# Kernel optimization log

Measured on AMD Instinct MI355X. Metric: run time of the kernel, lower is better.

## Reference

```python
import jax, jax.numpy as jnp
from jax import lax
import numpy as np

B = 32768
H = 7
W = 7
EMB = 64
NUM_ACTIONS = 7
HIDDEN = 128
CNN_OUT = 64 * 3 * 3  # 576, from 7x7 input through the conv/pool stack


def setup_inputs() -> dict:
    key = jax.random.key(0)
    ks = jax.random.split(key, 20)
    frame = jax.random.randint(ks[0], (2, B, H, W, 3), 0, 11, dtype=jnp.int32)
    carried_col = jax.random.randint(ks[1], (2, B, 1), 0, 6, dtype=jnp.int32)
    carried_obj = jax.random.randint(ks[2], (2, B, 1), 0, 11, dtype=jnp.int32)

    def w(k, shape):
        return (jax.random.normal(k, shape, jnp.float32) * 0.05)

    return {
        "frame": frame,
        "carried_col": carried_col,
        "carried_obj": carried_obj,
        "conv1_w": w(ks[3], (16, 3, 2, 2)),  "conv1_b": jnp.zeros((16,), jnp.float32),
        "conv2_w": w(ks[4], (32, 16, 2, 2)), "conv2_b": jnp.zeros((32,), jnp.float32),
        "conv3_w": w(ks[5], (64, 32, 2, 2)), "conv3_b": jnp.zeros((64,), jnp.float32),
        "proj_w": w(ks[6], (EMB, CNN_OUT + 2)), "proj_b": jnp.zeros((EMB,), jnp.float32),
        "h1_w": w(ks[7], (HIDDEN, EMB * 2 + 4)), "h1_b": jnp.zeros((HIDDEN,), jnp.float32),
        "ln_g": jnp.ones((HIDDEN,), jnp.float32), "ln_b": jnp.zeros((HIDDEN,), jnp.float32),
        "h2_w": w(ks[8], (HIDDEN, HIDDEN)), "h2_b": jnp.zeros((HIDDEN,), jnp.float32),
        "h3_w": w(ks[9], (NUM_ACTIONS, HIDDEN)), "h3_b": jnp.zeros((NUM_ACTIONS,), jnp.float32),
    }


def _conv(x, wgt, b):
    # Conv2d(kernel=2, padding=1), NCHW
    y = lax.conv_general_dilated(x, wgt, (1, 1), [(1, 1), (1, 1)],
                                 dimension_numbers=("NCHW", "OIHW", "NCHW"))
    return y + b[None, :, None, None]


def _maxpool2(x):
    # MaxPool2d(2): window 2, stride 2, floor (VALID)
    return lax.reduce_window(x, -jnp.inf, lax.max, (1, 1, 2, 2), (1, 1, 2, 2), "VALID")


def _encode(fr, cc, co, p):
    x = fr.transpose(0, 3, 1, 2).astype(jnp.float32)  # [B,3,H,W]
    x = _maxpool2(jax.nn.relu(_conv(x, p["conv1_w"], p["conv1_b"])))  # [B,16,4,4]
    x = _maxpool2(jax.nn.relu(_conv(x, p["conv2_w"], p["conv2_b"])))  # [B,32,2,2]
    x = jax.nn.relu(_conv(x, p["conv3_w"], p["conv3_b"]))             # [B,64,3,3]
    feats = x.reshape(x.shape[0], -1)                                  # [B,576]
    carried = jnp.concatenate([cc, co], axis=-1).astype(jnp.float32)   # [B,2]
    comb = jnp.concatenate([feats, carried], axis=1)                   # [B,578]
    return jax.nn.relu(comb @ p["proj_w"].T + p["proj_b"])            # [B,64]


def _dir_pos(fr):
    # vectorized first-match of frame[...,0]==10 in row-major order
    b = fr.shape[0]
    mask = (fr[..., 0] == 10).reshape(b, -1)             # [B, H*W]
    has = jnp.any(mask, axis=-1)                         # [B]
    idx = jnp.argmax(mask, axis=-1)                      # first True (row-major)
    y = idx // W
    x = idx % W
    ch2 = fr[..., 2].reshape(b, -1)
    d_raw = jnp.take_along_axis(ch2, idx[:, None], axis=1)[:, 0] % 4
    d = jnp.where(has, d_raw, 0)                         # [B] int
    pos = jnp.stack([y.astype(jnp.float32) / (H - 1),
                     x.astype(jnp.float32) / (W - 1)], axis=-1)
    pos = jnp.where(has[:, None], pos, jnp.float32(0.5))  # [B,2]
    return d, pos


def _forward(frame, carried_col, carried_obj, p):
    curr_f, next_f = frame[0], frame[1]
    curr_emb = _encode(curr_f, carried_col[0], carried_obj[0], p)
    next_emb = _encode(next_f, carried_col[1], carried_obj[1], p)
    cd, cpos = _dir_pos(curr_f)
    nd, npos = _dir_pos(next_f)
    delta = ((nd - cd + 4) % 4).astype(jnp.float32)
    angle = delta * (2.0 * 3.14159 / 4.0)  # matches source constant
    dir_delta = jnp.stack([jnp.sin(angle), jnp.cos(angle)], axis=-1)  # [B,2]
    pos_delta = npos - cpos                                           # [B,2]
    comb = jnp.concatenate([curr_emb, next_emb, dir_delta, pos_delta], axis=-1)  # [B,132]
    h = comb @ p["h1_w"].T + p["h1_b"]
    mu = h.mean(-1, keepdims=True)
    var = ((h - mu) ** 2).mean(-1, keepdims=True)
    h = (h - mu) * lax.rsqrt(var + 1e-5) * p["ln_g"] + p["ln_b"]
    h = jax.nn.relu(h)  # dropout = identity in eval
    h = jax.nn.relu(h @ p["h2_w"].T + p["h2_b"])
    return h @ p["h3_w"].T + p["h3_b"]  # [B, num_actions]


def reference(frame, carried_col, carried_obj,
              conv1_w, conv1_b, conv2_w, conv2_b, conv3_w, conv3_b,
              proj_w, proj_b, h1_w, h1_b, ln_g, ln_b,
              h2_w, h2_b, h3_w, h3_b):
    p = dict(conv1_w=conv1_w, conv1_b=conv1_b, conv2_w=conv2_w, conv2_b=conv2_b,
             conv3_w=conv3_w, conv3_b=conv3_b, proj_w=proj_w, proj_b=proj_b,
             h1_w=h1_w, h1_b=h1_b, ln_g=ln_g, ln_b=ln_b,
             h2_w=h2_w, h2_b=h2_b, h3_w=h3_w, h3_b=h3_b)
    return _forward(frame, carried_col, carried_obj, p)
```

## Files before the change

### kernel.cpp

```cpp
#include <hip/hip_runtime.h>
#include <hip/hip_bf16.h>

#define BATCH 32768
#define NELEM 65536

typedef unsigned short u16;
typedef unsigned int u32;
typedef __attribute__((ext_vector_type(8))) short bf16x8;
typedef __attribute__((ext_vector_type(4))) float f32x4;

__device__ __forceinline__ float bf2f(u16 u) {
    union { u32 u; float f; } c; c.u = ((u32)u) << 16; return c.f;
}
__device__ __forceinline__ u16 f2bf(float f) {
    union { float f; u32 u; } c; c.f = f;
    u32 x = c.u;
    u32 r = (x + 0x7fffu + ((x >> 16) & 1u)) >> 16;
    return (u16)r;
}

__global__ __launch_bounds__(256) void k0_prep(const float* __restrict__ pw,
        const float* __restrict__ w2, const float* __restrict__ w3,
        const float* __restrict__ h2w, const float* __restrict__ h1w,
        const float* __restrict__ w1,
        u16* __restrict__ pwT, u16* __restrict__ w2r, u16* __restrict__ w3r,
        u16* __restrict__ h2hi, u16* __restrict__ h2lo,
        u16* __restrict__ h1hi, u16* __restrict__ h1lo,
        u16* __restrict__ w1hi, u16* __restrict__ w1lo) {
    int idx = blockIdx.x * 256 + threadIdx.x;
    if (idx < 38912) {
        int j = idx / 608, kk = idx - j * 608;
        float v = 0.f;
        if (kk < 576) {
            int p = kk >> 6, oc = kk & 63;
            v = pw[j * 578 + oc * 9 + p];
        } else if (kk < 578) {
            v = pw[j * 578 + kk];
        }
        pwT[idx] = f2bf(v);
    } else if (idx < 40960) {
        int i = idx - 38912;
        int oc = i >> 6, rem = i & 63, tap = rem >> 4, ic = rem & 15;
        w2r[i] = f2bf(w2[oc * 64 + ic * 4 + tap]);
    } else if (idx < 49152) {
        int i = idx - 40960;
        int oc = i >> 7, rem = i & 127, tap = rem >> 5, ic = rem & 31;
        w3r[i] = f2bf(w3[oc * 128 + ic * 4 + tap]);
    } else if (idx < 65536) {
        int i = idx - 49152;
        float v = h2w[i];
        u16 hi = f2bf(v);
        h2hi[i] = hi;
        h2lo[i] = f2bf(v - bf2f(hi));
    } else if (idx < 86016) {
        int i = idx - 65536;
        int j = i / 160, k = i - j * 160;
        float v = (k < 132) ? h1w[j * 132 + k] : 0.f;
        u16 hi = f2bf(v);
        h1hi[i] = hi;
        h1lo[i] = f2bf(v - bf2f(hi));
    } else if (idx < 86528) {
        int i = idx - 86016;
        int oc = i >> 5, k = i & 31;
        int ky = k >> 4, kx = (k >> 3) & 1, c = k & 7;
        float v = (c < 3) ? w1[oc * 12 + c * 4 + ky * 2 + kx] : 0.f;
        u16 hi = f2bf(v);
        w1hi[i] = hi;
        w1lo[i] = f2bf(v - bf2f(hi));
    }
}

__global__ __launch_bounds__(256) void kconv_all(const int* __restrict__ frame,
        const u16* __restrict__ w1hi, const u16* __restrict__ w1lo,
        const float* __restrict__ b1,
        const u16* __restrict__ w2r, const float* __restrict__ b2,
        const u16* __restrict__ w3r, const float* __restrict__ b3,
        const int* __restrict__ ccol, const int* __restrict__ cobj,
        const u16* __restrict__ pwT, const float* __restrict__ pb,
        float* __restrict__ comb) {
    __shared__ u16 lds[24576];
    u16* p2L   = lds;
    u16* p1L   = lds + 4096;
    u16* frL   = lds + 12288;
    u16* featL = lds + 4096;
    int t = threadIdx.x;
    int l = t & 63;
    int wv = t >> 6;
    int col = l & 15;
    int kg = l >> 4;
    int e0 = blockIdx.x * 32;

    #pragma unroll
    for (int i = 0; i < 6; ++i) {
        int o = i * 256 + t;
        if (o < 1312) *(uint4*)(frL + o * 8) = make_uint4(0u, 0u, 0u, 0u);
    }

    {
        bf16x8 c1hi = *(const bf16x8*)(w1hi + col * 32 + kg * 8);
        bf16x8 c1lo = *(const bf16x8*)(w1lo + col * 32 + kg * 8);
        float c1b = b1[col];
        int ky1 = kg >> 1, kx1 = kg & 1;
        bool wr1 = (kg < 2);
        for (int h = 0; h < 2; ++h) {
            __syncthreads();
            const int* fbase = frame + (size_t)(e0 + h * 16) * 147;
            #pragma unroll
            for (int i = 0; i < 10; ++i) {
                int idx = i * 256 + t;
                if (idx < 2352) {
                    int le = idx / 147, r = idx - le * 147;
                    int cell = r / 3, c = r - cell * 3;
                    int y = cell / 7, x = cell - y * 7;
                    frL[le * 656 + (y + 1) * 72 + (x + 1) * 8 + c] = f2bf((float)fbase[idx]);
                }
            }
            __syncthreads();
            #pragma unroll
            for (int q = 0; q < 4; ++q) {
                int le = wv * 4 + q;
                const u16* eb = frL + le * 656;
                u16* op = p1L + (h * 16 + le) * 256;
                #pragma unroll
                for (int mt = 0; mt < 4; ++mt) {
                    int posA = mt * 16 + col;
                    int oy = posA >> 3, ox = posA & 7;
                    bf16x8 a = *(const bf16x8*)(eb + (oy + ky1) * 72 + (ox + kx1) * 8);
                    f32x4 acc = {0.f, 0.f, 0.f, 0.f};
                    acc = __builtin_amdgcn_mfma_f32_16x16x32_bf16(a, c1hi, acc, 0, 0, 0);
                    acc = __builtin_amdgcn_mfma_f32_16x16x32_bf16(a, c1lo, acc, 0, 0, 0);
                    float x0 = fmaxf(acc[0] + c1b, 0.f);
                    float x1 = fmaxf(acc[1] + c1b, 0.f);
                    float x2 = fmaxf(acc[2] + c1b, 0.f);
                    float x3 = fmaxf(acc[3] + c1b, 0.f);
                    float y0 = fmaxf(x0, x1);
                    float y1 = fmaxf(x2, x3);
                    float m0 = fmaxf(y0, __shfl_xor(y0, 32, 64));
                    float m1 = fmaxf(y1, __shfl_xor(y1, 32, 64));
                    if (wr1) {
                        op[(mt * 4 + kg * 2 + 0) * 16 + col] = f2bf(m0);
                        op[(mt * 4 + kg * 2 + 1) * 16 + col] = f2bf(m1);
                    }
                }
            }
        }
    }
    __syncthreads();

    {
        bf16x8 bfrag[2][2];
        #pragma unroll
        for (int s = 0; s < 2; ++s)
            #pragma unroll
            for (int nt = 0; nt < 2; ++nt)
                bfrag[s][nt] = *(const bf16x8*)(w2r + (nt * 16 + col) * 64 + s * 32 + kg * 8);
        float bias2[2] = { b2[col], b2[16 + col] };
        int oy = col >> 2, ox = col & 3;
        int aoff[2]; bool aok[2];
        #pragma unroll
        for (int s = 0; s < 2; ++s) {
            int tap = 2 * s + (kg >> 1);
            int ky = tap >> 1, kx = tap & 1;
            int iy = oy - 1 + ky, ix = ox - 1 + kx;
            aok[s] = (iy >= 0 && ix >= 0);
            aoff[s] = (iy * 4 + ix) * 16 + (kg & 1) * 8;
        }
        #pragma unroll
        for (int q = 0; q < 8; ++q) {
            int e = wv * 8 + q;
            const u16* pbase = p1L + e * 256;
            bf16x8 a0 = {0,0,0,0,0,0,0,0}, a1 = {0,0,0,0,0,0,0,0};
            if (aok[0]) a0 = *(const bf16x8*)(pbase + aoff[0]);
            if (aok[1]) a1 = *(const bf16x8*)(pbase + aoff[1]);
            f32x4 acc0 = {0.f,0.f,0.f,0.f}, acc1 = {0.f,0.f,0.f,0.f};
            acc0 = __builtin_amdgcn_mfma_f32_16x16x32_bf16(a0, bfrag[0][0], acc0, 0, 0, 0);
            acc1 = __builtin_amdgcn_mfma_f32_16x16x32_bf16(a0, bfrag[0][1], acc1, 0, 0, 0);
            acc0 = __builtin_amdgcn_mfma_f32_16x16x32_bf16(a1, bfrag[1][0], acc0, 0, 0, 0);
            acc1 = __builtin_amdgcn_mfma_f32_16x16x32_bf16(a1, bfrag[1][1], acc1, 0, 0, 0);
            #pragma unroll
            for (int nt = 0; nt < 2; ++nt) {
                f32x4 acc = nt ? acc1 : acc0;
                float b = bias2[nt];
                float m0 = fmaxf(fmaxf(acc[0] + b, 0.f), fmaxf(acc[1] + b, 0.f));
                float m1 = fmaxf(fmaxf(acc[2] + b, 0.f), fmaxf(acc[3] + b, 0.f));
                float p0 = fmaxf(m0, __shfl_xor(m0, 16, 64));
                float p1 = fmaxf(m1, __shfl_xor(m1, 16, 64));
                if ((kg & 1) == 0) {
                    int qq = (kg >> 1) * 2;
                    u16* op = p2L + e * 128 + nt * 16 + col;
                    op[qq * 32]       = f2bf(p0);
                    op[(qq + 1) * 32] = f2bf(p1);
                }
            }
        }
    }
    __syncthreads();

    int colhi = col >> 3, collo = col & 7;
    {
        bf16x8 bfrag[4][4];
        #pragma unroll
        for (int s = 0; s < 4; ++s)
            #pragma unroll
            for (int nt = 0; nt < 4; ++nt)
                bfrag[s][nt] = *(const bf16x8*)(w3r + (nt * 16 + col) * 128 + s * 32 + kg * 8);
        float bias[4];
        #pragma unroll
        for (int nt = 0; nt < 4; ++nt) bias[nt] = b3[nt * 16 + col];

        auto do_tile = [&](int i) {
            int m0 = i * 16;
            int m = m0 + col;
            u32 elem = (u32)(((unsigned long long)(u32)m * 954437177ull) >> 33);
            int p = m - (int)elem * 9;
            int oy = (p * 86) >> 8;
            int ox = p - 3 * oy;
            const u16* pbase = p2L + elem * 128 + kg * 8;
            f32x4 acc[4];
            #pragma unroll
            for (int nt = 0; nt < 4; ++nt) {
                acc[nt][0] = 0.f; acc[nt][1] = 0.f; acc[nt][2] = 0.f; acc[nt][3] = 0.f;
            }
            #pragma unroll
            for (int s = 0; s < 4; ++s) {
                int ky = s >> 1, kx = s & 1;
                int iy = oy - 1 + ky, ix = ox - 1 + kx;
                bf16x8 a = {0,0,0,0,0,0,0,0};
                if (iy >= 0 && iy <= 1 && ix >= 0 && ix <= 1)
                    a = *(const bf16x8*)(pbase + (iy * 2 + ix) * 32);
                #pragma unroll
                for (int nt = 0; nt < 4; ++nt)
                    acc[nt] = __builtin_amdgcn_mfma_f32_16x16x32_bf16(a, bfrag[s][nt], acc[nt], 0, 0, 0);
            }
            #pragma unroll
            for (int r = 0; r < 4; ++r) {
                int mr = m0 + kg * 4 + r;
                u32 er = (u32)(((unsigned long long)(u32)mr * 954437177ull) >> 33);
                int pr = mr - (int)er * 9;
                int e7 = (int)(er & 7u);
                u16* fb = featL + er * 640 + collo;
                #pragma unroll
                for (int nt = 0; nt < 4; ++nt) {
                    int blk = (pr * 8 + nt * 2 + colhi) ^ e7;
                    fb[blk * 8] = f2bf(fmaxf(acc[nt][r] + bias[nt], 0.f));
                }
            }
        };
        #pragma unroll
        for (int u = 0; u < 4; ++u) do_tile(wv + u * 4);
        if (wv < 2) do_tile(16 + wv);
    }
    if (t < 32) {
        union { u16 s[8]; uint4 q; } b;
        b.s[0] = f2bf((float)ccol[e0 + t]);
        b.s[1] = f2bf((float)cobj[e0 + t]);
        #pragma unroll
        for (int i = 2; i < 8; ++i) b.s[i] = 0;
        *(uint4*)(featL + t * 640 + (72 ^ (t & 7)) * 8) = b.q;
    }
    __syncthreads();

    int rh = wv & 1, nh = wv >> 1;
    int m0g = e0 + rh * 16;
    const u16* arowb = featL + (rh * 16 + col) * 640;
    int rx = col & 7;
    const u16* brow = pwT + (nh * 32 + col) * 608 + kg * 8;
    f32x4 acc0 = {0.f,0.f,0.f,0.f}, acc1 = {0.f,0.f,0.f,0.f};
    #pragma unroll
    for (int k0 = 0; k0 < 608; k0 += 32) {
        bf16x8 a;
        if (k0 + kg * 8 < 584) {
            int L = (k0 >> 3) + kg;
            a = *(const bf16x8*)(arowb + (L ^ rx) * 8);
        } else {
            #pragma unroll
            for (int j = 0; j < 8; ++j) a[j] = 0;
        }
        bf16x8 b0 = *(const bf16x8*)(brow + k0);
        bf16x8 b1 = *(const bf16x8*)(brow + 16 * 608 + k0);
        acc0 = __builtin_amdgcn_mfma_f32_16x16x32_bf16(a, b0, acc0, 0, 0, 0);
        acc1 = __builtin_amdgcn_mfma_f32_16x16x32_bf16(a, b1, acc1, 0, 0, 0);
    }
    float* outbase = (m0g < BATCH) ? (comb + (size_t)m0g * 160)
                                   : (comb + (size_t)(m0g - BATCH) * 160 + 64);
    #pragma unroll
    for (int nt = 0; nt < 2; ++nt) {
        int n = nh * 32 + nt * 16 + col;
        float pbv = pb[n];
        f32x4 acc = nt ? acc1 : acc0;
        #pragma unroll
        for (int r = 0; r < 4; ++r) {
            outbase[(kg * 4 + r) * 160 + n] = fmaxf(acc[r] + pbv, 0.f);
        }
    }
}

__global__ __launch_bounds__(256) void k5_extras(const int* __restrict__ frame,
        float* __restrict__ comb) {
    int b = blockIdx.x * 256 + threadIdx.x;
    int d[2]; float posy[2], posx[2];
    for (int f = 0; f < 2; ++f) {
        const int* fb = frame + (size_t)(f * BATCH + b) * 147;
        int idx = 49;
        for (int cell = 0; cell < 49; ++cell) {
            int v = fb[cell * 3];
            if (idx == 49 && v == 10) idx = cell;
        }
        if (idx < 49) {
            d[f] = fb[idx * 3 + 2] & 3;
            posy[f] = (float)(idx / 7) / 6.0f;
            posx[f] = (float)(idx % 7) / 6.0f;
        } else {
            d[f] = 0; posy[f] = 0.5f; posx[f] = 0.5f;
        }
    }
    int delta = (d[1] - d[0] + 4) & 3;
    const float ANG = (float)(2.0 * 3.14159 / 4.0);
    float angle = (float)delta * ANG;
    float4 o;
    o.x = sinf(angle);
    o.y = cosf(angle);
    o.z = posy[1] - posy[0];
    o.w = posx[1] - posx[0];
    float* cb = comb + (size_t)b * 160 + 128;
    *(float4*)cb = o;
    float4 z = make_float4(0.f, 0.f, 0.f, 0.f);
    #pragma unroll
    for (int i = 1; i < 8; ++i) *(float4*)(cb + i * 4) = z;
}

__device__ __forceinline__ void split8(const float* __restrict__ x,
                                       bf16x8& hi, bf16x8& lo) {
    #pragma unroll
    for (int j = 0; j < 8; ++j) {
        u16 h = f2bf(x[j]);
        hi[j] = (short)h;
        lo[j] = (short)f2bf(x[j] - bf2f(h));
    }
}

__global__ __launch_bounds__(256) void k6_h1_gemm(const float* __restrict__ in,
        const u16* __restrict__ whi, const u16* __restrict__ wlo,
        const float* __restrict__ bias, float* __restrict__ out) {
    int t = threadIdx.x;
    int l = t & 63;
    int col = l & 15;
    int kg = l >> 4;
    int m0 = blockIdx.x * 64 + (t >> 6) * 16;
    const float* arow = in + (size_t)(m0 + col) * 160 + kg * 8;
    const u16* bh = whi + col * 160 + kg * 8;
    const u16* bl = wlo + col * 160 + kg * 8;

    f32x4 acc[8];
    #pragma unroll
    for (int nt = 0; nt < 8; ++nt) {
        acc[nt][0] = 0.f; acc[nt][1] = 0.f; acc[nt][2] = 0.f; acc[nt][3] = 0.f;
    }
    #pragma unroll
    for (int s = 0; s < 5; ++s) {
        float x[8];
        #pragma unroll
        for (int j = 0; j < 8; ++j) x[j] = arow[s * 32 + j];
        bf16x8 ahi, alo;
        split8(x, ahi, alo);
        #pragma unroll
        for (int nt = 0; nt < 8; ++nt) {
            bf16x8 bhiF = *(const bf16x8*)(bh + nt * 2560 + s * 32);
            bf16x8 bloF = *(const bf16x8*)(bl + nt * 2560 + s * 32);
            acc[nt] = __builtin_amdgcn_mfma_f32_16x16x32_bf16(ahi, bhiF, acc[nt], 0, 0, 0);
            acc[nt] = __builtin_amdgcn_mfma_f32_16x16x32_bf16(alo, bhiF, acc[nt], 0, 0, 0);
            acc[nt] = __builtin_amdgcn_mfma_f32_16x16x32_bf16(ahi, bloF, acc[nt], 0, 0, 0);
        }
    }
    #pragma unroll
    for (int nt = 0; nt < 8; ++nt) {
        float bv = bias[nt * 16 + col];
        #pragma unroll
        for (int r = 0; r < 4; ++r) {
            int m = m0 + kg * 4 + r;
            out[m * 128 + nt * 16 + col] = acc[nt][r] + bv;
        }
    }
}

__global__ __launch_bounds__(256) void k6_ln(const float* __restrict__ h,
        const float* __restrict__ lng, const float* __restrict__ lnb,
        float* __restrict__ out) {
    int w = (blockIdx.x * 256 + threadIdx.x) >> 6;
    int l = threadIdx.x & 63;
    const float* row = h + (size_t)w * 128 + l * 2;
    float2 v = *(const float2*)row;
    float s = v.x + v.y;
    s += __shfl_xor(s, 1, 64);
    s += __shfl_xor(s, 2, 64);
    s += __shfl_xor(s, 4, 64);
    s += __shfl_xor(s, 8, 64);
    s += __shfl_xor(s, 16, 64);
    s += __shfl_xor(s, 32, 64);
    float mu = s * (1.0f / 128.0f);
    float d0 = v.x - mu, d1 = v.y - mu;
    float vs = d0 * d0 + d1 * d1;
    vs += __shfl_xor(vs, 1, 64);
    vs += __shfl_xor(vs, 2, 64);
    vs += __shfl_xor(vs, 4, 64);
    vs += __shfl_xor(vs, 8, 64);
    vs += __shfl_xor(vs, 16, 64);
    vs += __shfl_xor(vs, 32, 64);
    float rs = rsqrtf(vs * (1.0f / 128.0f) + 1e-5f);
    float2 o;
    o.x = fmaxf(d0 * rs * lng[l * 2]     + lnb[l * 2],     0.f);
    o.y = fmaxf(d1 * rs * lng[l * 2 + 1] + lnb[l * 2 + 1], 0.f);
    *(float2*)(out + (size_t)w * 128 + l * 2) = o;
}

__global__ __launch_bounds__(256) void k7_h2_mfma(const float* __restrict__ in,
        const u16* __restrict__ whi, const u16* __restrict__ wlo,
        const float* __restrict__ bias, float* __restrict__ out) {
    int t = threadIdx.x;
    int l = t & 63;
    int col = l & 15;
    int kg = l >> 4;
    int m0 = blockIdx.x * 64 + (t >> 6) * 16;
    const float* arow = in + (size_t)(m0 + col) * 128 + kg * 8;
    const u16* bh = whi + col * 128 + kg * 8;
    const u16* bl = wlo + col * 128 + kg * 8;

    f32x4 acc[8];
    #pragma unroll
    for (int nt = 0; nt < 8; ++nt) {
        acc[nt][0] = 0.f; acc[nt][1] = 0.f; acc[nt][2] = 0.f; acc[nt][3] = 0.f;
    }
    #pragma unroll
    for (int s = 0; s < 4; ++s) {
        float x[8];
        #pragma unroll
        for (int j = 0; j < 8; ++j) x[j] = arow[s * 32 + j];
        bf16x8 ahi, alo;
        split8(x, ahi, alo);
        #pragma unroll
        for (int nt = 0; nt < 8; ++nt) {
            bf16x8 bhiF = *(const bf16x8*)(bh + nt * 2048 + s * 32);
            bf16x8 bloF = *(const bf16x8*)(bl + nt * 2048 + s * 32);
            acc[nt] = __builtin_amdgcn_mfma_f32_16x16x32_bf16(ahi, bhiF, acc[nt], 0, 0, 0);
            acc[nt] = __builtin_amdgcn_mfma_f32_16x16x32_bf16(alo, bhiF, acc[nt], 0, 0, 0);
            acc[nt] = __builtin_amdgcn_mfma_f32_16x16x32_bf16(ahi, bloF, acc[nt], 0, 0, 0);
        }
    }
    #pragma unroll
    for (int nt = 0; nt < 8; ++nt) {
        float bv = bias[nt * 16 + col];
        #pragma unroll
        for (int r = 0; r < 4; ++r) {
            int m = m0 + kg * 4 + r;
            out[m * 128 + nt * 16 + col] = fmaxf(acc[nt][r] + bv, 0.f);
        }
    }
}

__global__ __launch_bounds__(256) void k8_h3(const float* __restrict__ in,
        const float* __restrict__ w, const float* __restrict__ bias,
        float* __restrict__ out) {
    int r = blockIdx.x * 256 + threadIdx.x;
    float acc[7];
    #pragma unroll
    for (int j = 0; j < 7; ++j) acc[j] = bias[j];
    const float* row = in + (size_t)r * 128;
    #pragma unroll 4
    for (int c = 0; c < 32; ++c) {
        float4 v = *(const float4*)(row + c * 4);
        #pragma unroll
        for (int j = 0; j < 7; ++j) {
            acc[j] += v.x * w[j * 128 + c * 4 + 0];
            acc[j] += v.y * w[j * 128 + c * 4 + 1];
            acc[j] += v.z * w[j * 128 + c * 4 + 2];
            acc[j] += v.w * w[j * 128 + c * 4 + 3];
        }
    }
    #pragma unroll
    for (int j = 0; j < 7; ++j) out[r * 7 + j] = acc[j];
}

extern "C" void kernel_launch(void* const* d_in, const int* in_sizes, int n_in,
                              void* d_out, int out_size, void* d_ws, size_t ws_size,
                              hipStream_t stream) {
    const int*   frame = (const int*)d_in[0];
    const int*   ccol  = (const int*)d_in[1];
    const int*   cobj  = (const int*)d_in[2];
    const float* w1    = (const float*)d_in[3];
    const float* b1    = (const float*)d_in[4];
    const float* w2    = (const float*)d_in[5];
    const float* b2    = (const float*)d_in[6];
    const float* w3    = (const float*)d_in[7];
    const float* b3    = (const float*)d_in[8];
    const float* pw    = (const float*)d_in[9];
    const float* pb    = (const float*)d_in[10];
    const float* h1w   = (const float*)d_in[11];
    const float* h1b   = (const float*)d_in[12];
    const float* lng   = (const float*)d_in[13];
    const float* lnb   = (const float*)d_in[14];
    const float* h2w   = (const float*)d_in[15];
    const float* h2b   = (const float*)d_in[16];
    const float* h3w   = (const float*)d_in[17];
    const float* h3b   = (const float*)d_in[18];
    float* out = (float*)d_out;

    char* ws = (char*)d_ws;
    float* comb     = (float*)(ws + 0);
    float* h1out    = (float*)(ws + 33554432);
    float* h2out    = (float*)(ws + 50331648);
    float* h1pre    = (float*)(ws + 95420416);
    u16*   pwT      = (u16*)(ws + 132120576);
    u16*   w2r      = (u16*)(ws + 132120576 + 131072);
    u16*   w3r      = (u16*)(ws + 132120576 + 139264);
    u16*   h2hi     = (u16*)(ws + 132120576 + 163840);
    u16*   h2lo     = (u16*)(ws + 132120576 + 196608);
    u16*   h1hi     = (u16*)(ws + 132120576 + 229376);
    u16*   h1lo     = (u16*)(ws + 132120576 + 270336);
    u16*   w1hi     = (u16*)(ws + 132120576 + 311296);
    u16*   w1lo     = (u16*)(ws + 132120576 + 312320);

    k0_prep<<<340, 256, 0, stream>>>(pw, w2, w3, h2w, h1w, w1,
                                     pwT, w2r, w3r, h2hi, h2lo, h1hi, h1lo,
                                     w1hi, w1lo);
    kconv_all<<<2048, 256, 0, stream>>>(frame, w1hi, w1lo, b1, w2r, b2,
                                        w3r, b3, ccol, cobj, pwT, pb, comb);
    k5_extras<<<128, 256, 0, stream>>>(frame, comb);
    k6_h1_gemm<<<512, 256, 0, stream>>>(comb, h1hi, h1lo, h1b, h1pre);
    k6_ln<<<8192, 256, 0, stream>>>(h1pre, lng, lnb, h1out);
    k7_h2_mfma<<<512, 256, 0, stream>>>(h1out, h2hi, h2lo, h2b, h2out);
    k8_h3<<<128, 256, 0, stream>>>(h2out, h3w, h3b, out);
}
```

Measured before the change: 255.9 us.

## Fuse h1 GEMM, LayerNorm, h2 GEMM and h3 head into one LDS-staged kernel

Replaces the four separate MLP-head kernels with a single kernel that keeps each 64-row tile in shared memory between stages. The h1 output, LayerNorm result and h2 output no longer round-trip through global memory, and three launches go away. In exchange the kernel holds about 33 KB of LDS per block and adds block barriers, which may lower occupancy. The final 7-wide head now runs on 4 threads per row, each computing two outputs.

```diff
diff --git a/kernel.cpp b/kernel.cpp
--- a/kernel.cpp
+++ b/kernel.cpp
@@ -339,145 +339,144 @@
     }
 }
 
-__global__ __launch_bounds__(256) void k6_h1_gemm(const float* __restrict__ in,
-        const u16* __restrict__ whi, const u16* __restrict__ wlo,
-        const float* __restrict__ bias, float* __restrict__ out) {
+__global__ __launch_bounds__(256) void kmlp(const float* __restrict__ comb,
+        const u16* __restrict__ h1hi, const u16* __restrict__ h1lo,
+        const float* __restrict__ h1b,
+        const float* __restrict__ lng, const float* __restrict__ lnb,
+        const u16* __restrict__ h2hi, const u16* __restrict__ h2lo,
+        const float* __restrict__ h2b,
+        const float* __restrict__ h3w, const float* __restrict__ h3b,
+        float* __restrict__ out) {
+    __shared__ float hL[64 * 132];
     int t = threadIdx.x;
     int l = t & 63;
     int col = l & 15;
     int kg = l >> 4;
-    int m0 = blockIdx.x * 64 + (t >> 6) * 16;
-    const float* arow = in + (size_t)(m0 + col) * 160 + kg * 8;
-    const u16* bh = whi + col * 160 + kg * 8;
-    const u16* bl = wlo + col * 160 + kg * 8;
-
-    f32x4 acc[8];
-    #pragma unroll
-    for (int nt = 0; nt < 8; ++nt) {
-        acc[nt][0] = 0.f; acc[nt][1] = 0.f; acc[nt][2] = 0.f; acc[nt][3] = 0.f;
-    }
-    #pragma unroll
-    for (int s = 0; s < 5; ++s) {
-        float x[8];
-        #pragma unroll
-        for (int j = 0; j < 8; ++j) x[j] = arow[s * 32 + j];
-        bf16x8 ahi, alo;
-        split8(x, ahi, alo);
+    int wv = t >> 6;
+    int mb = blockIdx.x * 64;
+
+    {
+        const float* arow = comb + (size_t)(mb + wv * 16 + col) * 160 + kg * 8;
+        const u16* bh = h1hi + col * 160 + kg * 8;
+        const u16* bl = h1lo + col * 160 + kg * 8;
+        f32x4 acc[8];
         #pragma unroll
         for (int nt = 0; nt < 8; ++nt) {
-            bf16x8 bhiF = *(const bf16x8*)(bh + nt * 2560 + s * 32);
-            bf16x8 bloF = *(const bf16x8*)(bl + nt * 2560 + s * 32);
-            acc[nt] = __builtin_amdgcn_mfma_f32_16x16x32_bf16(ahi, bhiF, acc[nt], 0, 0, 0);
-            acc[nt] = __builtin_amdgcn_mfma_f32_16x16x32_bf16(alo, bhiF, acc[nt], 0, 0, 0);
-            acc[nt] = __builtin_amdgcn_mfma_f32_16x16x32_bf16(ahi, bloF, acc[nt], 0, 0, 0);
-        }
-    }
-    #pragma unroll
-    for (int nt = 0; nt < 8; ++nt) {
-        float bv = bias[nt * 16 + col];
-        #pragma unroll
-        for (int r = 0; r < 4; ++r) {
-            int m = m0 + kg * 4 + r;
-            out[m * 128 + nt * 16 + col] = acc[nt][r] + bv;
-        }
-    }
-}
-
-__global__ __launch_bounds__(256) void k6_ln(const float* __restrict__ h,
-        const float* __restrict__ lng, const float* __restrict__ lnb,
-        float* __restrict__ out) {
-    int w = (blockIdx.x * 256 + threadIdx.x) >> 6;
-    int l = threadIdx.x & 63;
-    const float* row = h + (size_t)w * 128 + l * 2;
-    float2 v = *(const float2*)row;
-    float s = v.x + v.y;
-    s += __shfl_xor(s, 1, 64);
-    s += __shfl_xor(s, 2, 64);
-    s += __shfl_xor(s, 4, 64);
-    s += __shfl_xor(s, 8, 64);
-    s += __shfl_xor(s, 16, 64);
-    s += __shfl_xor(s, 32, 64);
-    float mu = s * (1.0f / 128.0f);
-    float d0 = v.x - mu, d1 = v.y - mu;
-    float vs = d0 * d0 + d1 * d1;
-    vs += __shfl_xor(vs, 1, 64);
-    vs += __shfl_xor(vs, 2, 64);
-    vs += __shfl_xor(vs, 4, 64);
-    vs += __shfl_xor(vs, 8, 64);
-    vs += __shfl_xor(vs, 16, 64);
-    vs += __shfl_xor(vs, 32, 64);
-    float rs = rsqrtf(vs * (1.0f / 128.0f) + 1e-5f);
-    float2 o;
-    o.x = fmaxf(d0 * rs * lng[l * 2]     + lnb[l * 2],     0.f);
-    o.y = fmaxf(d1 * rs * lng[l * 2 + 1] + lnb[l * 2 + 1], 0.f);
-    *(float2*)(out + (size_t)w * 128 + l * 2) = o;
-}
-
-__global__ __launch_bounds__(256) void k7_h2_mfma(const float* __restrict__ in,
-        const u16* __restrict__ whi, const u16* __restrict__ wlo,
-        const float* __restrict__ bias, float* __restrict__ out) {
-    int t = threadIdx.x;
-    int l = t & 63;
-    int col = l & 15;
-    int kg = l >> 4;
-    int m0 = blockIdx.x * 64 + (t >> 6) * 16;
-    const float* arow = in + (size_t)(m0 + col) * 128 + kg * 8;
-    const u16* bh = whi + col * 128 + kg * 8;
-    const u16* bl = wlo + col * 128 + kg * 8;
-
-    f32x4 acc[8];
-    #pragma unroll
-    for (int nt = 0; nt < 8; ++nt) {
-        acc[nt][0] = 0.f; acc[nt][1] = 0.f; acc[nt][2] = 0.f; acc[nt][3] = 0.f;
-    }
-    #pragma unroll
-    for (int s = 0; s < 4; ++s) {
-        float x[8];
-        #pragma unroll
-        for (int j = 0; j < 8; ++j) x[j] = arow[s * 32 + j];
-        bf16x8 ahi, alo;
-        split8(x, ahi, alo);
+            acc[nt][0] = 0.f; acc[nt][1] = 0.f; acc[nt][2] = 0.f; acc[nt][3] = 0.f;
+        }
+        #pragma unroll
+        for (int s = 0; s < 5; ++s) {
+            float x[8];
+            #pragma unroll
+            for (int j = 0; j < 8; ++j) x[j] = arow[s * 32 + j];
+            bf16x8 ahi, alo;
+            split8(x, ahi, alo);
+            #pragma unroll
+            for (int nt = 0; nt < 8; ++nt) {
+                bf16x8 bhiF = *(const bf16x8*)(bh + nt * 2560 + s * 32);
+                bf16x8 bloF = *(const bf16x8*)(bl + nt * 2560 + s * 32);
+                acc[nt] = __builtin_amdgcn_mfma_f32_16x16x32_bf16(ahi, bhiF, acc[nt], 0, 0, 0);
+                acc[nt] = __builtin_amdgcn_mfma_f32_16x16x32_bf16(alo, bhiF, acc[nt], 0, 0, 0);
+                acc[nt] = __builtin_amdgcn_mfma_f32_16x16x32_bf16(ahi, bloF, acc[nt], 0, 0, 0);
+            }
+        }
         #pragma unroll
         for (int nt = 0; nt < 8; ++nt) {
-            bf16x8 bhiF = *(const bf16x8*)(bh + nt * 2048 + s * 32);
-            bf16x8 bloF = *(const bf16x8*)(bl + nt * 2048 + s * 32);
-            acc[nt] = __builtin_amdgcn_mfma_f32_16x16x32_bf16(ahi, bhiF, acc[nt], 0, 0, 0);
-            acc[nt] = __builtin_amdgcn_mfma_f32_16x16x32_bf16(alo, bhiF, acc[nt], 0, 0, 0);
-            acc[nt] = __builtin_amdgcn_mfma_f32_16x16x32_bf16(ahi, bloF, acc[nt], 0, 0, 0);
-        }
-    }
-    #pragma unroll
-    for (int nt = 0; nt < 8; ++nt) {
-        float bv = bias[nt * 16 + col];
-        #pragma unroll
-        for (int r = 0; r < 4; ++r) {
-            int m = m0 + kg * 4 + r;
-            out[m * 128 + nt * 16 + col] = fmaxf(acc[nt][r] + bv, 0.f);
-        }
-    }
-}
-
-__global__ __launch_bounds__(256) void k8_h3(const float* __restrict__ in,
-        const float* __restrict__ w, const float* __restrict__ bias,
-        float* __restrict__ out) {
-    int r = blockIdx.x * 256 + threadIdx.x;
-    float acc[7];
-    #pragma unroll
-    for (int j = 0; j < 7; ++j) acc[j] = bias[j];
-    const float* row = in + (size_t)r * 128;
-    #pragma unroll 4
-    for (int c = 0; c < 32; ++c) {
-        float4 v = *(const float4*)(row + c * 4);
-        #pragma unroll
-        for (int j = 0; j < 7; ++j) {
-            acc[j] += v.x * w[j * 128 + c * 4 + 0];
-            acc[j] += v.y * w[j * 128 + c * 4 + 1];
-            acc[j] += v.z * w[j * 128 + c * 4 + 2];
-            acc[j] += v.w * w[j * 128 + c * 4 + 3];
-        }
-    }
-    #pragma unroll
-    for (int j = 0; j < 7; ++j) out[r * 7 + j] = acc[j];
+            float bv = h1b[nt * 16 + col];
+            #pragma unroll
+            for (int r = 0; r < 4; ++r)
+                hL[(wv * 16 + kg * 4 + r) * 132 + nt * 16 + col] = acc[nt][r] + bv;
+        }
+    }
+    __syncthreads();
+
+    for (int rr = 0; rr < 16; ++rr) {
+        float* rp = hL + (wv * 16 + rr) * 132 + l * 2;
+        float2 v = *(const float2*)rp;
+        float s = v.x + v.y;
+        s += __shfl_xor(s, 1, 64);
+        s += __shfl_xor(s, 2, 64);
+        s += __shfl_xor(s, 4, 64);
+        s += __shfl_xor(s, 8, 64);
+        s += __shfl_xor(s, 16, 64);
+        s += __shfl_xor(s, 32, 64);
+        float mu = s * (1.0f / 128.0f);
+        float d0 = v.x - mu, d1 = v.y - mu;
+        float vs = d0 * d0 + d1 * d1;
+        vs += __shfl_xor(vs, 1, 64);
+        vs += __shfl_xor(vs, 2, 64);
+        vs += __shfl_xor(vs, 4, 64);
+        vs += __shfl_xor(vs, 8, 64);
+        vs += __shfl_xor(vs, 16, 64);
+        vs += __shfl_xor(vs, 32, 64);
+        float rs = rsqrtf(vs * (1.0f / 128.0f) + 1e-5f);
+        float2 o;
+        o.x = fmaxf(d0 * rs * lng[l * 2]     + lnb[l * 2],     0.f);
+        o.y = fmaxf(d1 * rs * lng[l * 2 + 1] + lnb[l * 2 + 1], 0.f);
+        *(float2*)rp = o;
+    }
+    __syncthreads();
+
+    {
+        const float* arow = hL + (wv * 16 + col) * 132 + kg * 8;
+        const u16* bh = h2hi + col * 128 + kg * 8;
+        const u16* bl = h2lo + col * 128 + kg * 8;
+        f32x4 acc[8];
+        #pragma unroll
+        for (int nt = 0; nt < 8; ++nt) {
+            acc[nt][0] = 0.f; acc[nt][1] = 0.f; acc[nt][2] = 0.f; acc[nt][3] = 0.f;
+        }
+        #pragma unroll
+        for (int s = 0; s < 4; ++s) {
+            float x[8];
+            #pragma unroll
+            for (int j = 0; j < 8; ++j) x[j] = arow[s * 32 + j];
+            bf16x8 ahi, alo;
+            split8(x, ahi, alo);
+            #pragma unroll
+            for (int nt = 0; nt < 8; ++nt) {
+                bf16x8 bhiF = *(const bf16x8*)(bh + nt * 2048 + s * 32);
+                bf16x8 bloF = *(const bf16x8*)(bl + nt * 2048 + s * 32);
+                acc[nt] = __builtin_amdgcn_mfma_f32_16x16x32_bf16(ahi, bhiF, acc[nt], 0, 0, 0);
+                acc[nt] = __builtin_amdgcn_mfma_f32_16x16x32_bf16(alo, bhiF, acc[nt], 0, 0, 0);
+                acc[nt] = __builtin_amdgcn_mfma_f32_16x16x32_bf16(ahi, bloF, acc[nt], 0, 0, 0);
+            }
+        }
+        #pragma unroll
+        for (int nt = 0; nt < 8; ++nt) {
+            float bv = h2b[nt * 16 + col];
+            #pragma unroll
+            for (int r = 0; r < 4; ++r)
+                hL[(wv * 16 + kg * 4 + r) * 132 + nt * 16 + col] = fmaxf(acc[nt][r] + bv, 0.f);
+        }
+    }
+    __syncthreads();
+
+    {
+        int row = t >> 2, jq = t & 3, j0 = jq * 2;
+        const float* rp = hL + row * 132;
+        float a0 = h3b[j0];
+        float a1 = (jq < 3) ? h3b[j0 + 1] : 0.f;
+        #pragma unroll 4
+        for (int c = 0; c < 32; ++c) {
+            float4 v = *(const float4*)(rp + c * 4);
+            const float* wr0 = h3w + j0 * 128 + c * 4;
+            a0 += v.x * wr0[0];
+            a0 += v.y * wr0[1];
+            a0 += v.z * wr0[2];
+            a0 += v.w * wr0[3];
+            if (jq < 3) {
+                const float* wr1 = h3w + (j0 + 1) * 128 + c * 4;
+                a1 += v.x * wr1[0];
+                a1 += v.y * wr1[1];
+                a1 += v.z * wr1[2];
+                a1 += v.w * wr1[3];
+            }
+        }
+        float* ob = out + (size_t)(mb + row) * 7;
+        ob[j0] = a0;
+        if (jq < 3) ob[j0 + 1] = a1;
+    }
 }
 
 extern "C" void kernel_launch(void* const* d_in, const int* in_sizes, int n_in,
@@ -506,9 +505,6 @@
 
     char* ws = (char*)d_ws;
     float* comb     = (float*)(ws + 0);
-    float* h1out    = (float*)(ws + 33554432);
-    float* h2out    = (float*)(ws + 50331648);
-    float* h1pre    = (float*)(ws + 95420416);
     u16*   pwT      = (u16*)(ws + 132120576);
     u16*   w2r      = (u16*)(ws + 132120576 + 131072);
     u16*   w3r      = (u16*)(ws + 132120576 + 139264);
@@ -525,8 +521,6 @@
     kconv_all<<<2048, 256, 0, stream>>>(frame, w1hi, w1lo, b1, w2r, b2,
                                         w3r, b3, ccol, cobj, pwT, pb, comb);
     k5_extras<<<128, 256, 0, stream>>>(frame, comb);
-    k6_h1_gemm<<<512, 256, 0, stream>>>(comb, h1hi, h1lo, h1b, h1pre);
-    k6_ln<<<8192, 256, 0, stream>>>(h1pre, lng, lnb, h1out);
-    k7_h2_mfma<<<512, 256, 0, stream>>>(h1out, h2hi, h2lo, h2b, h2out);
-    k8_h3<<<128, 256, 0, stream>>>(h2out, h3w, h3b, out);
-}
+    kmlp<<<512, 256, 0, stream>>>(comb, h1hi, h1lo, h1b, lng, lnb,
+                                  h2hi, h2lo, h2b, h3w, h3b, out);
+}
```

New measurement: 248.8 us. 2.8% less time.
